# Optimization experiments

Hardware: AMD Instinct MI355X
Metric: run time of the kernel (lower is better)

Reference implementation:

```python
import jax, jax.numpy as jnp
import numpy as np

DIM = 192
HEADS = 8
EPS = 1e-12

def conv2d(x, w, groups=1, padding='SAME'):
    return jax.lax.conv_general_dilated(
        x, w, window_strides=(1, 1), padding=padding,
        dimension_numbers=('NCHW', 'OIHW', 'NCHW'),
        feature_group_count=groups)

def setup_inputs() -> dict:
    key = jax.random.key(0)
    ks = jax.random.split(key, 6)
    b, c, h, w = 8, DIM, 128, 128
    x = jax.random.normal(ks[0], (b, c, h, w), dtype=jnp.float32)
    # depthwise 3x3 conv on x (groups=dim): OIHW with I=1
    w_dw = jax.random.normal(ks[1], (DIM, 1, 3, 3), dtype=jnp.float32) * 0.1
    # 1x1 qkv projection
    w_qkv = jax.random.normal(ks[2], (DIM * 3, DIM, 1, 1), dtype=jnp.float32) * (1.0 / np.sqrt(DIM))
    # depthwise 3x3 on qkv (groups=3*dim)
    w_qkvdw = jax.random.normal(ks[3], (DIM * 3, 1, 3, 3), dtype=jnp.float32) * 0.1
    # 1x1 output projection
    w_proj = jax.random.normal(ks[4], (DIM, DIM, 1, 1), dtype=jnp.float32) * (1.0 / np.sqrt(DIM))
    temperature = jnp.ones((HEADS, 1, 1), dtype=jnp.float32)
    rescale = jnp.ones((HEADS, 1), dtype=jnp.float32)
    return {"x": x, "w_dw": w_dw, "w_qkv": w_qkv, "w_qkvdw": w_qkvdw,
            "w_proj": w_proj, "temperature": temperature, "rescale": rescale}

def l2norm_lastdim(t):
    # matches F.normalize(t, dim=-1, eps=1e-12)
    n = jnp.sqrt(jnp.sum(t * t, axis=-1, keepdims=True))
    return t / jnp.maximum(n, EPS)

def reference(x, w_dw, w_qkv, w_qkvdw, w_proj, temperature, rescale):
    b, c, h, w = x.shape
    heads = HEADS
    c_head = c // heads
    # variance (unbiased, like torch.var default) of depthwise-conv features over H,W
    xd = conv2d(x, w_dw, groups=c)                      # [b,c,h,w]
    var = jnp.var(xd, axis=(-2, -1), ddof=1)            # [b,c]
    var = var.reshape(b, heads, c_head)                 # [b,head,c_head]
    # qkv: 1x1 conv then depthwise 3x3
    qkv = conv2d(conv2d(x, w_qkv), w_qkvdw, groups=3 * c)  # [b,3c,h,w]
    q, k, v = jnp.split(qkv, 3, axis=1)
    def to_heads(t):
        return t.reshape(b, heads, c_head, h * w)       # b head c (h w)
    q, k, v = to_heads(q), to_heads(k), to_heads(v)
    q = l2norm_lastdim(q)
    k = l2norm_lastdim(k)
    # channel attention: [b,head,c_head,c_head]
    attn = jnp.einsum('bhcn,bhdn->bhcd', q, k) * temperature
    # diagonal bias from variance, scaled per-head
    diag = rescale * var                                # [b,head,c_head]
    attn = attn + jnp.einsum('bhc,cd->bhcd', diag, jnp.eye(c_head, dtype=attn.dtype))
    attn = jax.nn.softmax(attn, axis=-1)
    out = jnp.einsum('bhcd,bhdn->bhcn', attn, v)        # [b,head,c_head,hw]
    out = out.reshape(b, c, h, w)
    return conv2d(out, w_proj)
```

## Files before the change

### kernel.cpp

```cpp
#include <hip/hip_runtime.h>
#include <hip/hip_bf16.h>

typedef unsigned short ushort_t;
typedef __bf16 bf16x8 __attribute__((ext_vector_type(8)));
typedef float f32x4 __attribute__((ext_vector_type(4)));
typedef unsigned short us8 __attribute__((ext_vector_type(8)));
typedef unsigned short us4 __attribute__((ext_vector_type(4)));

#define HW 16384
#define CDIM 192
#define QKVC 576

static __device__ __forceinline__ float b2f(unsigned short u) {
    union { unsigned int i; float f; } cv; cv.i = ((unsigned int)u) << 16; return cv.f;
}
static __device__ __forceinline__ unsigned short f2b(float f) {
    union { __bf16 h; unsigned short u; } cv; cv.h = (__bf16)f; return cv.u;
}

__global__ __launch_bounds__(256) void k_cvt(const float* __restrict__ src,
                                             ushort_t* __restrict__ dst, int n8) {
    int i = blockIdx.x * 256 + threadIdx.x;
    if (i >= n8) return;
    f32x4 a = *(const f32x4*)&src[i * 8];
    f32x4 b = *(const f32x4*)&src[i * 8 + 4];
    us8 o;
#pragma unroll
    for (int e = 0; e < 4; ++e) { o[e] = f2b(a[e]); o[4 + e] = f2b(b[e]); }
    *(us8*)&dst[i * 8] = o;
}

__global__ __launch_bounds__(256) void k_dwvar(const float* __restrict__ x,
                                               const float* __restrict__ wdw,
                                               float* __restrict__ var,
                                               ushort_t* __restrict__ xb) {
    __shared__ __align__(16) float pl[128 * 132 + 132];
    __shared__ float red[8];
    int bc = blockIdx.x;
    int c = bc % CDIM;
    const float* xp = x + (size_t)bc * HW;
    ushort_t* xbp = xb + (size_t)bc * HW;
    int t = threadIdx.x;
#pragma unroll
    for (int i = 0; i < 16; ++i) {
        int gi = t + i * 256;
        int y = gi >> 5, xq = (gi & 31) << 2;
        f32x4 v4 = *(const f32x4*)&xp[gi * 4];
        *(f32x4*)&pl[y * 132 + xq] = v4;
        us4 b4;
#pragma unroll
        for (int j = 0; j < 4; ++j) b4[j] = f2b(v4[j]);
        *(us4*)&xbp[gi * 4] = b4;
    }
    if (t < 33) { f32x4 zz = {0.f, 0.f, 0.f, 0.f}; *(f32x4*)&pl[16896 + t * 4] = zz; }
    float w[9];
#pragma unroll
    for (int j = 0; j < 9; ++j) w[j] = wdw[c * 9 + j];
    __syncthreads();

    int y = t >> 1, xs = (t & 1) * 64;
    int yb0 = (y > 0)   ? (y - 1) * 132 : 16896;
    int yb1 = y * 132;
    int yb2 = (y < 127) ? (y + 1) * 132 : 16896;
    float l0 = 0.f, l1 = 0.f, l2 = 0.f;
    if (xs != 0) { l0 = pl[yb0 + 63]; l1 = pl[yb1 + 63]; l2 = pl[yb2 + 63]; }
    float s1 = 0.f, s2 = 0.f;
#pragma unroll
    for (int g = 0; g < 8; ++g) {
        int x0 = xs + g * 8;
        float e0[10], e1[10], e2[10];
        e0[0] = l0; e1[0] = l1; e2[0] = l2;
        f32x4 a0 = *(const f32x4*)&pl[yb0 + x0], b0 = *(const f32x4*)&pl[yb0 + x0 + 4];
        f32x4 a1 = *(const f32x4*)&pl[yb1 + x0], b1 = *(const f32x4*)&pl[yb1 + x0 + 4];
        f32x4 a2 = *(const f32x4*)&pl[yb2 + x0], b2 = *(const f32x4*)&pl[yb2 + x0 + 4];
#pragma unroll
        for (int j = 0; j < 4; ++j) {
            e0[1 + j] = a0[j]; e0[5 + j] = b0[j];
            e1[1 + j] = a1[j]; e1[5 + j] = b1[j];
            e2[1 + j] = a2[j]; e2[5 + j] = b2[j];
        }
        float r0 = 0.f, r1 = 0.f, r2 = 0.f;
        if (x0 + 8 < 128) { r0 = pl[yb0 + x0 + 8]; r1 = pl[yb1 + x0 + 8]; r2 = pl[yb2 + x0 + 8]; }
        e0[9] = r0; e1[9] = r1; e2[9] = r2;
#pragma unroll
        for (int j = 0; j < 8; ++j) {
            float o = e0[j] * w[0] + e0[j + 1] * w[1] + e0[j + 2] * w[2]
                    + e1[j] * w[3] + e1[j + 1] * w[4] + e1[j + 2] * w[5]
                    + e2[j] * w[6] + e2[j + 1] * w[7] + e2[j + 2] * w[8];
            s1 += o; s2 += o * o;
        }
        l0 = e0[8]; l1 = e1[8]; l2 = e2[8];
    }
#pragma unroll
    for (int off = 32; off; off >>= 1) { s1 += __shfl_xor(s1, off); s2 += __shfl_xor(s2, off); }
    int wv = t >> 6;
    if ((t & 63) == 0) { red[wv * 2] = s1; red[wv * 2 + 1] = s2; }
    __syncthreads();
    if (t == 0) {
        float S1 = red[0] + red[2] + red[4] + red[6];
        float S2 = red[1] + red[3] + red[5] + red[7];
        var[bc] = (S2 - S1 * S1 * (1.0f / 16384.f)) * (1.0f / 16383.f);
    }
}

__global__ __launch_bounds__(256) void k_dwqkv(const ushort_t* __restrict__ qkvraw,
                                               const float* __restrict__ wqd,
                                               ushort_t* __restrict__ qkvd,
                                               float* __restrict__ ssq) {
    __shared__ __align__(16) ushort_t pl[128 * 136 + 136];
    __shared__ float red[4];
    int bo = blockIdx.x;
    int o = bo % QKVC, b = bo / QKVC;
    const ushort_t* xp = qkvraw + (size_t)bo * HW;
    ushort_t* op = qkvd + (size_t)bo * HW;
    int t = threadIdx.x;
#pragma unroll
    for (int i = 0; i < 8; ++i) {
        int gi = t + i * 256;
        int y = gi >> 4, xo = (gi & 15) * 8;
        *(us8*)&pl[y * 136 + xo] = *(const us8*)&xp[gi * 8];
    }
    if (t < 17) { us8 zz = {}; *(us8*)&pl[17408 + t * 8] = zz; }
    float w[9];
#pragma unroll
    for (int j = 0; j < 9; ++j) w[j] = wqd[o * 9 + j];
    __syncthreads();

    int y = t >> 1, xs = (t & 1) * 64;
    int yb0 = (y > 0)   ? (y - 1) * 136 : 17408;
    int yb1 = y * 136;
    int yb2 = (y < 127) ? (y + 1) * 136 : 17408;
    float l0 = 0.f, l1 = 0.f, l2 = 0.f;
    if (xs != 0) { l0 = b2f(pl[yb0 + 63]); l1 = b2f(pl[yb1 + 63]); l2 = b2f(pl[yb2 + 63]); }
    float s2 = 0.f;
#pragma unroll
    for (int g = 0; g < 8; ++g) {
        int x0 = xs + g * 8;
        us8 v0 = *(const us8*)&pl[yb0 + x0];
        us8 v1 = *(const us8*)&pl[yb1 + x0];
        us8 v2 = *(const us8*)&pl[yb2 + x0];
        float r0 = 0.f, r1 = 0.f, r2 = 0.f;
        if (x0 + 8 < 128) { r0 = b2f(pl[yb0 + x0 + 8]); r1 = b2f(pl[yb1 + x0 + 8]); r2 = b2f(pl[yb2 + x0 + 8]); }
        float e0[10], e1[10], e2[10];
        e0[0] = l0; e1[0] = l1; e2[0] = l2;
#pragma unroll
        for (int j = 0; j < 8; ++j) { e0[j + 1] = b2f(v0[j]); e1[j + 1] = b2f(v1[j]); e2[j + 1] = b2f(v2[j]); }
        e0[9] = r0; e1[9] = r1; e2[9] = r2;
        us8 ob;
#pragma unroll
        for (int j = 0; j < 8; ++j) {
            float ov = e0[j] * w[0] + e0[j + 1] * w[1] + e0[j + 2] * w[2]
                     + e1[j] * w[3] + e1[j + 1] * w[4] + e1[j + 2] * w[5]
                     + e2[j] * w[6] + e2[j + 1] * w[7] + e2[j + 2] * w[8];
            unsigned short bits = f2b(ov);
            ob[j] = bits;
            float rv = b2f(bits);
            s2 += rv * rv;
        }
        *(us8*)&op[(size_t)y * 128 + x0] = ob;
        l0 = e0[8]; l1 = e1[8]; l2 = e2[8];
    }
    if (o < 2 * CDIM) {
#pragma unroll
        for (int off = 32; off; off >>= 1) s2 += __shfl_xor(s2, off);
        int wv = t >> 6;
        if ((t & 63) == 0) red[wv] = s2;
        __syncthreads();
        if (t == 0) ssq[b * 384 + o] = red[0] + red[1] + red[2] + red[3];
    }
}

template<int CF>
__global__ __launch_bounds__(256) void k_gemm(const ushort_t* __restrict__ Av, long sAb,
                                              const ushort_t* __restrict__ Bv, long sBb,
                                              void* __restrict__ Cv, long sCb, int K) {
    __shared__ __align__(16) ushort_t As[192 * 64];
    __shared__ __align__(16) ushort_t Bs[128 * 64];
    int t = threadIdx.x;
    int wv = t >> 6, lane = t & 63, quad = lane >> 4, l15 = lane & 15;
    size_t aoff = (size_t)blockIdx.z * sAb + (size_t)blockIdx.y * 192 * K;
    size_t boff = (size_t)blockIdx.z * sBb + (size_t)blockIdx.x * 128;
    size_t coff = (size_t)blockIdx.z * sCb + (size_t)blockIdx.y * 192 * HW + (size_t)blockIdx.x * 128;
    f32x4 acc[24] = {};
    int bkr = t >> 3, bn0 = (t & 7) * 16, tlow = t & 7;
    for (int kk = 0; kk < K; kk += 64) {
#pragma unroll
        for (int i = 0; i < 6; ++i) {
            int s = t + i * 256;
            int row = s >> 3, kc = (s & 7) * 8;
            int kcs = kc ^ ((row & 7) * 8);
            *(uint4*)&As[row * 64 + kcs] = *(const uint4*)&Av[aoff + (size_t)row * K + kk + kc];
        }
        const ushort_t* Bp = Bv + boff;
#pragma unroll
        for (int h = 0; h < 2; ++h) {
            int krow = bkr + h * 32;
            int gk = krow >> 3, klo = krow & 7;
            us8 t0 = *(const us8*)&Bp[(size_t)(kk + krow) * HW + bn0];
            us8 t1 = *(const us8*)&Bp[(size_t)(kk + krow) * HW + bn0 + 8];
#pragma unroll
            for (int e = 0; e < 8; ++e) {
                int col = ((gk ^ tlow ^ e) << 3) + klo;
                Bs[(bn0 + e) * 64 + col] = t0[e];
                Bs[(bn0 + 8 + e) * 64 + col] = t1[e];
            }
        }
        __syncthreads();
#pragma unroll
        for (int s = 0; s < 2; ++s) {
            int r0 = wv * 16 + l15, r1 = 64 + r0, r2 = 128 + r0;
            int ko = s * 32 + quad * 8;
            bf16x8 af0 = *(const bf16x8*)&As[r0 * 64 + (ko ^ ((r0 & 7) * 8))];
            bf16x8 af1 = *(const bf16x8*)&As[r1 * 64 + (ko ^ ((r1 & 7) * 8))];
            bf16x8 af2 = *(const bf16x8*)&As[r2 * 64 + (ko ^ ((r2 & 7) * 8))];
#pragma unroll
            for (int tc = 0; tc < 8; ++tc) {
                int n = tc * 16 + l15;
                int g = (s * 4 + quad) ^ ((tc ^ l15) & 7);
                bf16x8 bfr = *(const bf16x8*)&Bs[n * 64 + (g << 3)];
                acc[tc]      = __builtin_amdgcn_mfma_f32_16x16x32_bf16(af0, bfr, acc[tc],      0, 0, 0);
                acc[8 + tc]  = __builtin_amdgcn_mfma_f32_16x16x32_bf16(af1, bfr, acc[8 + tc],  0, 0, 0);
                acc[16 + tc] = __builtin_amdgcn_mfma_f32_16x16x32_bf16(af2, bfr, acc[16 + tc], 0, 0, 0);
            }
        }
        __syncthreads();
    }
#pragma unroll
    for (int rt = 0; rt < 3; ++rt)
#pragma unroll
        for (int tc = 0; tc < 8; ++tc)
#pragma unroll
            for (int r = 0; r < 4; ++r) {
                int row = rt * 64 + wv * 16 + quad * 4 + r;
                size_t idx = coff + (size_t)row * HW + tc * 16 + l15;
                if (CF) ((float*)Cv)[idx] = acc[rt * 8 + tc][r];
                else    ((ushort_t*)Cv)[idx] = f2b(acc[rt * 8 + tc][r]);
            }
}

__global__ __launch_bounds__(256) void k_gram(const ushort_t* __restrict__ qkvd,
                                              float* __restrict__ G) {
    __shared__ __align__(16) ushort_t qs[24 * 264];
    __shared__ __align__(16) ushort_t ks[24 * 264];
    int bh = blockIdx.y;
    int b = bh >> 3, h = bh & 7;
    int t = threadIdx.x, wv = t >> 6, lane = t & 63, quad = lane >> 4, l15 = lane & 15;
    const ushort_t* qb = qkvd + (size_t)b * 9437184 + (size_t)(h * 24) * HW;
    const ushort_t* kp = qb + (size_t)CDIM * HW;
    f32x4 a00 = {}, a01 = {}, a10 = {}, a11 = {};
    bf16x8 z = {};
    bool hi = (l15 < 8);
    int kbase0 = blockIdx.x * 2048;
    for (int sub = 0; sub < 8; ++sub) {
        int kbase = kbase0 + sub * 256;
#pragma unroll
        for (int j = 0; j < 3; ++j) {
            int gi = t + j * 256;
            int row = gi >> 5, c8 = (gi & 31) * 8;
            *(us8*)&qs[row * 264 + c8] = *(const us8*)&qb[(size_t)row * HW + kbase + c8];
            *(us8*)&ks[row * 264 + c8] = *(const us8*)&kp[(size_t)row * HW + kbase + c8];
        }
        __syncthreads();
#pragma unroll
        for (int s = 0; s < 2; ++s) {
            int ko = (wv * 2 + s) * 32 + quad * 8;
            bf16x8 qa0 = *(const bf16x8*)&qs[l15 * 264 + ko];
            bf16x8 qa1 = hi ? *(const bf16x8*)&qs[(16 + l15) * 264 + ko] : z;
            bf16x8 kb0 = *(const bf16x8*)&ks[l15 * 264 + ko];
            bf16x8 kb1 = hi ? *(const bf16x8*)&ks[(16 + l15) * 264 + ko] : z;
            a00 = __builtin_amdgcn_mfma_f32_16x16x32_bf16(qa0, kb0, a00, 0, 0, 0);
            a01 = __builtin_amdgcn_mfma_f32_16x16x32_bf16(qa0, kb1, a01, 0, 0, 0);
            a10 = __builtin_amdgcn_mfma_f32_16x16x32_bf16(qa1, kb0, a10, 0, 0, 0);
            a11 = __builtin_amdgcn_mfma_f32_16x16x32_bf16(qa1, kb1, a11, 0, 0, 0);
        }
        __syncthreads();
    }
    float* Gp = G + (size_t)bh * 576;
#pragma unroll
    for (int r = 0; r < 4; ++r) {
        int r0 = quad * 4 + r, r1 = 16 + quad * 4 + r;
        int c0 = l15, c1 = 16 + l15;
        atomicAdd(&Gp[r0 * 24 + c0], a00[r]);
        if (c1 < 24) atomicAdd(&Gp[r0 * 24 + c1], a01[r]);
        if (r1 < 24) atomicAdd(&Gp[r1 * 24 + c0], a10[r]);
        if (r1 < 24 && c1 < 24) atomicAdd(&Gp[r1 * 24 + c1], a11[r]);
    }
}

__global__ __launch_bounds__(256) void k_smweff(const float* __restrict__ G,
                                                const float* __restrict__ ssq,
                                                const float* __restrict__ var,
                                                const float* __restrict__ wproj,
                                                const float* __restrict__ temp,
                                                const float* __restrict__ resc,
                                                ushort_t* __restrict__ Weff) {
    int b = blockIdx.x, t = threadIdx.x;
    __shared__ float P[8 * 24 * 24];
    __shared__ float snq[192], snk[192];
    if (t < 192) {
        snq[t] = fmaxf(sqrtf(ssq[b * 384 + t]), 1e-12f);
        snk[t] = fmaxf(sqrtf(ssq[b * 384 + 192 + t]), 1e-12f);
    }
    __syncthreads();
    if (t < 192) {
        int h = t / 24, c = t % 24;
        float tmpv = temp[h];
        float dvar = resc[h] * var[b * 192 + t];
        const float* Gp = G + (size_t)(b * 8 + h) * 576 + c * 24;
        float inq = tmpv / snq[t];
        float lg[24]; float mx = -1e30f;
#pragma unroll
        for (int d = 0; d < 24; ++d) {
            float v = Gp[d] * inq / snk[h * 24 + d];
            if (d == c) v += dvar;
            lg[d] = v; mx = fmaxf(mx, v);
        }
        float sum = 0.f;
#pragma unroll
        for (int d = 0; d < 24; ++d) { float e = __expf(lg[d] - mx); lg[d] = e; sum += e; }
        float inv = 1.f / sum;
#pragma unroll
        for (int d = 0; d < 24; ++d) P[(h * 24 + c) * 24 + d] = lg[d] * inv;
    }
    __syncthreads();
#pragma unroll
    for (int i = 0; i < 6; ++i) {
        int idx = t + (blockIdx.y * 6 + i) * 256;
        int co = idx / 192, hd = idx % 192;
        int h2 = hd / 24, d = hd % 24;
        float a = 0.f;
#pragma unroll
        for (int c2 = 0; c2 < 24; ++c2)
            a += wproj[co * 192 + h2 * 24 + c2] * P[(h2 * 24 + c2) * 24 + d];
        Weff[(size_t)b * 36864 + idx] = f2b(a);
    }
}

extern "C" void kernel_launch(void* const* d_in, const int* in_sizes, int n_in,
                              void* d_out, int out_size, void* d_ws, size_t ws_size,
                              hipStream_t stream) {
    const float* x      = (const float*)d_in[0];
    const float* wdw    = (const float*)d_in[1];
    const float* wqkv   = (const float*)d_in[2];
    const float* wqkvdw = (const float*)d_in[3];
    const float* wproj  = (const float*)d_in[4];
    const float* temp   = (const float*)d_in[5];
    const float* resc   = (const float*)d_in[6];
    float* out = (float*)d_out;

    char* ws = (char*)d_ws;
    ushort_t* qkvraw = (ushort_t*)ws;
    ushort_t* qkvd   = (ushort_t*)(ws + 150994944);
    char* small = ws + 301989888;
    float* var  = (float*)small;
    float* ssq  = (float*)(small + 6144);
    float* G    = (float*)(small + 6144 + 12288);
    ushort_t* Weff = (ushort_t*)(small + 6144 + 12288 + 147456);

    ushort_t* xb  = qkvd;
    ushort_t* wqb = qkvd + 60000000;

    (void)hipMemsetAsync(G, 0, 147456, stream);
    k_cvt<<<dim3(54), dim3(256), 0, stream>>>(wqkv, wqb, 13824);
    k_dwvar<<<dim3(1536), dim3(256), 0, stream>>>(x, wdw, var, xb);
    k_gemm<0><<<dim3(128, 3, 8), dim3(256), 0, stream>>>(wqb, 0L, xb, 3145728L, qkvraw, 9437184L, 192);
    k_dwqkv<<<dim3(4608), dim3(256), 0, stream>>>(qkvraw, wqkvdw, qkvd, ssq);
    k_gram<<<dim3(8, 64), dim3(256), 0, stream>>>(qkvd, G);
    k_smweff<<<dim3(8, 24), dim3(256), 0, stream>>>(G, ssq, var, wproj, temp, resc, Weff);
    k_gemm<1><<<dim3(128, 1, 8), dim3(256), 0, stream>>>(Weff, 36864L, qkvd + (size_t)384 * HW, 9437184L, out, 3145728L, 192);
}
```

Baseline: 405.9 us.

## Prefetch next B tile into registers and stage GEMM epilogue through LDS

The GEMM kernel now loads the next K-slice of B into registers while the MFMA loop for the current slice runs, so global load latency overlaps compute. The output epilogue is staged through shared memory: accumulators are written to LDS, then copied out with 16-byte vector stores instead of scattered 2- or 4-byte stores. Shared memory is merged into one 48KB buffer reused for the epilogue. The cost is extra registers for the prefetch, extra syncs, and LDS round trips in the epilogue.

```diff
diff --git a/kernel.cpp b/kernel.cpp
--- a/kernel.cpp
+++ b/kernel.cpp
@@ -174,8 +174,9 @@
 __global__ __launch_bounds__(256) void k_gemm(const ushort_t* __restrict__ Av, long sAb,
                                               const ushort_t* __restrict__ Bv, long sBb,
                                               void* __restrict__ Cv, long sCb, int K) {
-    __shared__ __align__(16) ushort_t As[192 * 64];
-    __shared__ __align__(16) ushort_t Bs[128 * 64];
+    __shared__ __align__(16) char smem[49152];
+    ushort_t* As = (ushort_t*)smem;
+    ushort_t* Bs = (ushort_t*)(smem + 24576);
     int t = threadIdx.x;
     int wv = t >> 6, lane = t & 63, quad = lane >> 4, l15 = lane & 15;
     size_t aoff = (size_t)blockIdx.z * sAb + (size_t)blockIdx.y * 192 * K;
@@ -183,7 +184,15 @@
     size_t coff = (size_t)blockIdx.z * sCb + (size_t)blockIdx.y * 192 * HW + (size_t)blockIdx.x * 128;
     f32x4 acc[24] = {};
     int bkr = t >> 3, bn0 = (t & 7) * 16, tlow = t & 7;
-    for (int kk = 0; kk < K; kk += 64) {
+    int gk0 = bkr >> 3, klo = bkr & 7;
+    const ushort_t* Bp = Bv + boff;
+    us8 pb0 = *(const us8*)&Bp[(size_t)bkr * HW + bn0];
+    us8 pb1 = *(const us8*)&Bp[(size_t)bkr * HW + bn0 + 8];
+    us8 pb2 = *(const us8*)&Bp[(size_t)(bkr + 32) * HW + bn0];
+    us8 pb3 = *(const us8*)&Bp[(size_t)(bkr + 32) * HW + bn0 + 8];
+    int nIter = K >> 6;
+    for (int it = 0; it < nIter; ++it) {
+        int kk = it << 6;
 #pragma unroll
         for (int i = 0; i < 6; ++i) {
             int s = t + i * 256;
@@ -191,21 +200,23 @@
             int kcs = kc ^ ((row & 7) * 8);
             *(uint4*)&As[row * 64 + kcs] = *(const uint4*)&Av[aoff + (size_t)row * K + kk + kc];
         }
-        const ushort_t* Bp = Bv + boff;
-#pragma unroll
-        for (int h = 0; h < 2; ++h) {
-            int krow = bkr + h * 32;
-            int gk = krow >> 3, klo = krow & 7;
-            us8 t0 = *(const us8*)&Bp[(size_t)(kk + krow) * HW + bn0];
-            us8 t1 = *(const us8*)&Bp[(size_t)(kk + krow) * HW + bn0 + 8];
-#pragma unroll
-            for (int e = 0; e < 8; ++e) {
-                int col = ((gk ^ tlow ^ e) << 3) + klo;
-                Bs[(bn0 + e) * 64 + col] = t0[e];
-                Bs[(bn0 + 8 + e) * 64 + col] = t1[e];
-            }
-        }
-        __syncthreads();
+#pragma unroll
+        for (int e = 0; e < 8; ++e) {
+            int col0 = ((gk0 ^ tlow ^ e) << 3) + klo;
+            Bs[(bn0 + e) * 64 + col0] = pb0[e];
+            Bs[(bn0 + 8 + e) * 64 + col0] = pb1[e];
+            int col1 = (((gk0 + 4) ^ tlow ^ e) << 3) + klo;
+            Bs[(bn0 + e) * 64 + col1] = pb2[e];
+            Bs[(bn0 + 8 + e) * 64 + col1] = pb3[e];
+        }
+        __syncthreads();
+        if (it + 1 < nIter) {
+            const ushort_t* Bn = &Bp[(size_t)(kk + 64) * HW];
+            pb0 = *(const us8*)&Bn[(size_t)bkr * HW + bn0];
+            pb1 = *(const us8*)&Bn[(size_t)bkr * HW + bn0 + 8];
+            pb2 = *(const us8*)&Bn[(size_t)(bkr + 32) * HW + bn0];
+            pb3 = *(const us8*)&Bn[(size_t)(bkr + 32) * HW + bn0 + 8];
+        }
 #pragma unroll
         for (int s = 0; s < 2; ++s) {
             int r0 = wv * 16 + l15, r1 = 64 + r0, r2 = 128 + r0;
@@ -225,17 +236,43 @@
         }
         __syncthreads();
     }
-#pragma unroll
-    for (int rt = 0; rt < 3; ++rt)
-#pragma unroll
-        for (int tc = 0; tc < 8; ++tc)
-#pragma unroll
-            for (int r = 0; r < 4; ++r) {
-                int row = rt * 64 + wv * 16 + quad * 4 + r;
-                size_t idx = coff + (size_t)row * HW + tc * 16 + l15;
-                if (CF) ((float*)Cv)[idx] = acc[rt * 8 + tc][r];
-                else    ((ushort_t*)Cv)[idx] = f2b(acc[rt * 8 + tc][r]);
+    if (CF == 0) {
+        ushort_t* Ct = (ushort_t*)smem;
+#pragma unroll
+        for (int rt = 0; rt < 3; ++rt)
+#pragma unroll
+            for (int tc = 0; tc < 8; ++tc)
+#pragma unroll
+                for (int r = 0; r < 4; ++r)
+                    Ct[(rt * 64 + wv * 16 + quad * 4 + r) * 128 + tc * 16 + l15] = f2b(acc[rt * 8 + tc][r]);
+        __syncthreads();
+        ushort_t* Co = (ushort_t*)Cv;
+#pragma unroll
+        for (int i = 0; i < 12; ++i) {
+            int s = t + i * 256;
+            int row = s >> 4, c8 = (s & 15) * 8;
+            *(us8*)&Co[coff + (size_t)row * HW + c8] = *(us8*)&Ct[row * 128 + c8];
+        }
+    } else {
+        float* Cf = (float*)smem;
+        float* Co = (float*)Cv;
+#pragma unroll
+        for (int rt = 0; rt < 3; ++rt) {
+            if (rt) __syncthreads();
+#pragma unroll
+            for (int tc = 0; tc < 8; ++tc)
+#pragma unroll
+                for (int r = 0; r < 4; ++r)
+                    Cf[(wv * 16 + quad * 4 + r) * 128 + tc * 16 + l15] = acc[rt * 8 + tc][r];
+            __syncthreads();
+#pragma unroll
+            for (int i = 0; i < 8; ++i) {
+                int s = t + i * 256;
+                int row = s >> 5, c4 = (s & 31) * 4;
+                *(f32x4*)&Co[coff + (size_t)(rt * 64 + row) * HW + c4] = *(f32x4*)&Cf[row * 128 + c4];
             }
+        }
+    }
 }
 
 __global__ __launch_bounds__(256) void k_gram(const ushort_t* __restrict__ qkvd,
```

New measurement: 373.4 us. -8.0%, faster.
